# Kernel optimization log

Hardware: AMD Instinct MI355X
Metric: run time of the kernel (lower is better)

## Reference

```python
import jax, jax.numpy as jnp
import numpy as np

B, D = 4096, 256          # event batch, message dim
N_NODES = 100000
N_COMM = 2000             # community_max_num
M = 128                   # max_member_num
N_ACTIVE = 1500           # currently active communities (community_index)


def setup_inputs() -> dict:
    key = jax.random.key(0)
    ks = jax.random.split(key, 8)
    return {
        "unique_message": jax.random.normal(ks[0], (B, D), jnp.float32),
        "member_score": jax.random.uniform(ks[1], (N_COMM, M), jnp.float32),
        "timestamps": jax.random.uniform(ks[2], (B,), jnp.float32) * 1e4,
        "nodes": jax.random.randint(ks[3], (B,), 0, N_NODES),
        "node2community": jax.random.randint(ks[4], (N_NODES,), 0, N_COMM),
        "community2node": jax.random.randint(ks[5], (N_COMM, M), 0, N_NODES),
        "member_num": jax.random.randint(ks[6], (N_COMM,), 1, M + 1),
        "community_index": jax.random.randint(ks[7], (N_ACTIVE,), 0, N_COMM),
    }


def reference(unique_message, member_score, timestamps, nodes,
              node2community, community2node, member_num, community_index):
    # community of each event node: [B]
    cids = node2community[nodes]
    # use_index: event's community is among active communities (== .any in torch code)
    use = (cids[None, :] == community_index[:, None]).any(axis=0)  # [B]

    # Ragged per-community gather, expressed as padded+masked dense ops.
    ms = member_score[cids]          # [B, M] scores of the event's community members
    mnum = member_num[cids]          # [B]   valid member count per event
    pos = jnp.arange(M)
    valid = (pos[None, :] < mnum[:, None]) & use[:, None]  # [B, M] mask = ragged prefix

    # outer product member_score[:mnum] x message  (torch.mm(score.view(-1,1), msg.view(1,-1)))
    messages = jnp.where(valid[:, :, None],
                         ms[:, :, None] * unique_message[:, None, :],
                         0.0)                                # [B, M, D]
    upd_nodes = jnp.where(valid, community2node[cids], -1)   # [B, M] (-1 = pad)
    upd_ts = jnp.where(valid, timestamps[:, None], 0.0)      # [B, M]
    return messages, upd_nodes, upd_ts
```

## Files before the change

### kernel.cpp

```cpp
#include <hip/hip_runtime.h>
#include <hip/hip_bf16.h>


typedef float f32x4 __attribute__((ext_vector_type(4)));

constexpr int Dc = 256;
constexpr int Mc = 128;

__global__ __launch_bounds__(256) void topk_main_spec(
    const float* __restrict__ unique_message,
    const float* __restrict__ member_score,
    const float* __restrict__ timestamps,
    const int*   __restrict__ nodes,
    const int*   __restrict__ node2community,
    const int*   __restrict__ community2node,
    const int*   __restrict__ member_num,
    const int*   __restrict__ community_index,
    int n_active,
    float* __restrict__ out_msgs,
    float* __restrict__ out_nodes,
    float* __restrict__ out_ts)
{
    const int b    = blockIdx.x;
    const int tid  = threadIdx.x;
    const int lane = tid & 63;
    const int r    = tid >> 6;

    __shared__ float s_score[Mc];

    const f32x4 m4 = reinterpret_cast<const f32x4*>(
        unique_message + (size_t)b * Dc)[lane];

    const int   cid  = node2community[nodes[b]];
    const int   mnum = member_num[cid];
    const float tsb  = timestamps[b];

    if (tid < Mc) s_score[tid] = member_score[(size_t)cid * Mc + tid];

    bool f = false;
    for (int i = lane; i < n_active; i += 64)
        f |= (community_index[i] == cid);
    const bool use = __any(f);
    const int  mlim = use ? mnum : 0;

    if (tid < Mc) {
        const bool valid = tid < mlim;
        const float vn = valid ? (float)community2node[(size_t)cid * Mc + tid]
                               : -1.0f;
        __builtin_nontemporal_store(vn,  &out_nodes[(size_t)b * Mc + tid]);
        __builtin_nontemporal_store(valid ? tsb : 0.0f,
                                    &out_ts[(size_t)b * Mc + tid]);
    }

    __syncthreads();

    f32x4* __restrict__ outm = reinterpret_cast<f32x4*>(
        out_msgs + (size_t)b * Mc * Dc) + (size_t)r * (32 * 64) + lane;

    const int m0 = r * 32;
#pragma unroll
    for (int k = 0; k < 32; ++k) {
        const int m = m0 + k;
        const float s = (m < mlim) ? s_score[m] : 0.0f;
        f32x4 o;
        o.x = s * m4.x; o.y = s * m4.y; o.z = s * m4.z; o.w = s * m4.w;
        __builtin_nontemporal_store(o, outm + (size_t)k * 64);
    }
}

extern "C" void kernel_launch(void* const* d_in, const int* in_sizes, int n_in,
                              void* d_out, int out_size, void* d_ws, size_t ws_size,
                              hipStream_t stream) {
    const float* unique_message  = (const float*)d_in[0];
    const float* member_score    = (const float*)d_in[1];
    const float* timestamps      = (const float*)d_in[2];
    const int*   nodes           = (const int*)d_in[3];
    const int*   node2community  = (const int*)d_in[4];
    const int*   community2node  = (const int*)d_in[5];
    const int*   member_num      = (const int*)d_in[6];
    const int*   community_index = (const int*)d_in[7];

    const int B        = in_sizes[2];
    const int N_COMM   = in_sizes[6];
    const int M        = in_sizes[1] / N_COMM;
    const int D        = in_sizes[0] / B;
    const int N_ACTIVE = in_sizes[7];

    float* out_msgs  = (float*)d_out;
    float* out_nodes = out_msgs + (size_t)B * M * D;
    float* out_ts    = out_nodes + (size_t)B * M;

    (void)d_ws; (void)ws_size; (void)n_in; (void)out_size; (void)M; (void)D;

    topk_main_spec<<<B, 256, 0, stream>>>(
        unique_message, member_score, timestamps, nodes,
        node2community, community2node, member_num,
        community_index, N_ACTIVE,
        out_msgs, out_nodes, out_ts);
}
```

Measured before the change: 95.84 us.

## Process two events per block with software-pipelined prefetch of next event

Each block now handles two events (strided by grid size), with the next event's community lookup, active-set scan and message row loaded while the current event's outputs are written. Scores are double-buffered in shared memory. The aim is to hide the dependent gather latency behind the large store stream and to halve the block count. It adds an extra barrier, and B must be divisible by EPB.

```diff
diff --git a/kernel.cpp b/kernel.cpp
--- a/kernel.cpp
+++ b/kernel.cpp
@@ -4,8 +4,9 @@
 
 typedef float f32x4 __attribute__((ext_vector_type(4)));
 
-constexpr int Dc = 256;
-constexpr int Mc = 128;
+constexpr int Dc  = 256;
+constexpr int Mc  = 128;
+constexpr int EPB = 2;
 
 __global__ __launch_bounds__(256) void topk_main_spec(
     const float* __restrict__ unique_message,
@@ -21,50 +22,74 @@
     float* __restrict__ out_nodes,
     float* __restrict__ out_ts)
 {
-    const int b    = blockIdx.x;
     const int tid  = threadIdx.x;
     const int lane = tid & 63;
     const int r    = tid >> 6;
+    const int nblk = gridDim.x;
 
-    __shared__ float s_score[Mc];
+    __shared__ float s_score[2][Mc];
 
-    const f32x4 m4 = reinterpret_cast<const f32x4*>(
-        unique_message + (size_t)b * Dc)[lane];
+    int e = blockIdx.x;
 
-    const int   cid  = node2community[nodes[b]];
-    const int   mnum = member_num[cid];
-    const float tsb  = timestamps[b];
-
-    if (tid < Mc) s_score[tid] = member_score[(size_t)cid * Mc + tid];
-
-    bool f = false;
-    for (int i = lane; i < n_active; i += 64)
-        f |= (community_index[i] == cid);
-    const bool use = __any(f);
-    const int  mlim = use ? mnum : 0;
-
-    if (tid < Mc) {
-        const bool valid = tid < mlim;
-        const float vn = valid ? (float)community2node[(size_t)cid * Mc + tid]
-                               : -1.0f;
-        __builtin_nontemporal_store(vn,  &out_nodes[(size_t)b * Mc + tid]);
-        __builtin_nontemporal_store(valid ? tsb : 0.0f,
-                                    &out_ts[(size_t)b * Mc + tid]);
+    int   cid  = node2community[nodes[e]];
+    int   mnum = member_num[cid];
+    float ts   = timestamps[e];
+    f32x4 m4   = reinterpret_cast<const f32x4*>(
+                     unique_message + (size_t)e * Dc)[lane];
+    {
+        bool f = false;
+        for (int i = lane; i < n_active; i += 64)
+            f |= (community_index[i] == cid);
+        mnum = __any(f) ? mnum : 0;
     }
-
+    if (tid < Mc) s_score[0][tid] = member_score[(size_t)cid * Mc + tid];
     __syncthreads();
 
-    f32x4* __restrict__ outm = reinterpret_cast<f32x4*>(
-        out_msgs + (size_t)b * Mc * Dc) + (size_t)r * (32 * 64) + lane;
+    int buf = 0;
+#pragma unroll
+    for (int ei = 0; ei < EPB; ++ei) {
+        int   en = e, cidn = cid, mlimn = 0;
+        float tsn = 0.0f;
+        f32x4 m4n = m4;
+        if (ei + 1 < EPB) {
+            en   = e + nblk;
+            cidn = node2community[nodes[en]];
+            const int mnumn = member_num[cidn];
+            tsn  = timestamps[en];
+            m4n  = reinterpret_cast<const f32x4*>(
+                       unique_message + (size_t)en * Dc)[lane];
+            bool fn = false;
+            for (int i = lane; i < n_active; i += 64)
+                fn |= (community_index[i] == cidn);
+            mlimn = __any(fn) ? mnumn : 0;
+        }
 
-    const int m0 = r * 32;
+        if (tid < Mc) {
+            const bool  valid = tid < mnum;
+            const float vn = valid
+                ? (float)community2node[(size_t)cid * Mc + tid] : -1.0f;
+            __builtin_nontemporal_store(vn,  &out_nodes[(size_t)e * Mc + tid]);
+            __builtin_nontemporal_store(valid ? ts : 0.0f,
+                                        &out_ts[(size_t)e * Mc + tid]);
+        }
+
+        if (ei + 1 < EPB && tid < Mc)
+            s_score[buf ^ 1][tid] = member_score[(size_t)cidn * Mc + tid];
+
+        f32x4* __restrict__ outm = reinterpret_cast<f32x4*>(
+            out_msgs + (size_t)e * Mc * Dc) + (size_t)r * (32 * 64) + lane;
+        const int m0 = r * 32;
 #pragma unroll
-    for (int k = 0; k < 32; ++k) {
-        const int m = m0 + k;
-        const float s = (m < mlim) ? s_score[m] : 0.0f;
-        f32x4 o;
-        o.x = s * m4.x; o.y = s * m4.y; o.z = s * m4.z; o.w = s * m4.w;
-        __builtin_nontemporal_store(o, outm + (size_t)k * 64);
+        for (int k = 0; k < 32; ++k) {
+            const float s = (m0 + k < mnum) ? s_score[buf][m0 + k] : 0.0f;
+            f32x4 o;
+            o.x = s * m4.x; o.y = s * m4.y; o.z = s * m4.z; o.w = s * m4.w;
+            __builtin_nontemporal_store(o, outm + (size_t)k * 64);
+        }
+
+        __syncthreads();
+
+        e = en; cid = cidn; mnum = mlimn; ts = tsn; m4 = m4n; buf ^= 1;
     }
 }
 
@@ -92,7 +117,7 @@
 
     (void)d_ws; (void)ws_size; (void)n_in; (void)out_size; (void)M; (void)D;
 
-    topk_main_spec<<<B, 256, 0, stream>>>(
+    topk_main_spec<<<B / EPB, 256, 0, stream>>>(
         unique_message, member_score, timestamps, nodes,
         node2community, community2node, member_num,
         community_index, N_ACTIVE,
```

Result: slower. 99.96 us (+4.3%).
